# Performance work log

Hardware: AMD Instinct MI355X
Metric: run time of the kernel (lower is better)

Reference implementation:

```python
import jax, jax.numpy as jnp
import numpy as np

B, T, C = 128, 512, 512
EPS = 1e-5


def setup_inputs() -> dict:
    key = jax.random.key(0)
    ks = jax.random.split(key, 12)
    s_tri = 1.0 / np.sqrt(T)   # rough torch Linear init scale (per-row fan-in varies; fixed for simplicity)
    s_fc1 = 1.0 / np.sqrt(C)
    s_fc2 = 1.0 / np.sqrt(2 * C)
    return {
        "inputs": jax.random.normal(ks[0], (B, T, C), dtype=jnp.float32),
        "ln1_w": jnp.ones((T, C), jnp.float32),
        "ln1_b": jnp.zeros((T, C), jnp.float32),
        "ln2_w": jnp.ones((T, C), jnp.float32),
        "ln2_b": jnp.zeros((T, C), jnp.float32),
        # Row s of triu_W corresponds to nn.Linear(s+1, 1); entries j> s are masked in reference().
        "triu_W": jax.random.uniform(ks[1], (T, T), jnp.float32, -s_tri, s_tri),
        "triu_b": jax.random.uniform(ks[2], (T,), jnp.float32, -s_tri, s_tri),
        "fc1_W": jax.random.uniform(ks[3], (2 * C, C), jnp.float32, -s_fc1, s_fc1),
        "fc1_b": jax.random.uniform(ks[4], (2 * C,), jnp.float32, -s_fc1, s_fc1),
        "fc2_W": jax.random.uniform(ks[5], (C, 2 * C), jnp.float32, -s_fc2, s_fc2),
        "fc2_b": jax.random.uniform(ks[6], (C,), jnp.float32, -s_fc2, s_fc2),
    }


def _layernorm_2d(x, w, b):
    # torch nn.LayerNorm((T, C)): normalize jointly over the last TWO dims.
    mu = jnp.mean(x, axis=(-2, -1), keepdims=True)
    var = jnp.var(x, axis=(-2, -1), keepdims=True)
    return (x - mu) * jax.lax.rsqrt(var + EPS) * w + b


def reference(inputs, ln1_w, ln1_b, ln2_w, ln2_b, triu_W, triu_b, fc1_W, fc1_b, fc2_W, fc2_b):
    x = _layernorm_2d(inputs, ln1_w, ln1_b)                       # [B,T,C]
    # TriU time mixer on x.mT ([B,C,T]): out[..., s] = sum_{t<=s} W[s,t]*x[..., t] + b[s]
    Wm = jnp.tril(triu_W)                                          # causal mask
    xm = jnp.einsum('btc,st->bsc', x, Wm) + triu_b[None, :, None]  # [B,T,C] (already back-transposed)
    x2 = _layernorm_2d(xm + inputs, ln2_w, ln2_b)                  # [B,T,C]
    h = jax.nn.gelu(jnp.einsum('btc,hc->bth', x2, fc1_W) + fc1_b, approximate=False)
    y = jnp.einsum('bth,ch->btc', h, fc2_W) + fc2_b
    return x2 + y
```

## Files before the change

### kernel.cpp

```cpp
#include <hip/hip_runtime.h>
#include <hip/hip_fp8.h>
#include <cstdint>

typedef unsigned short u16;
typedef unsigned char u8;
typedef __attribute__((ext_vector_type(8))) short s16x8;
typedef __attribute__((ext_vector_type(4))) float f32x4;
typedef __attribute__((ext_vector_type(8))) unsigned short u16x8;
typedef __attribute__((ext_vector_type(4))) unsigned short u16x4;
typedef __attribute__((ext_vector_type(2))) long l64x2;

#define B_ 128
#define T_ 512
#define C_ 512
#define TC 262144

static __device__ __forceinline__ float bf2f(u16 u) {
  union { unsigned int i; float f; } v; v.i = ((unsigned int)u) << 16; return v.f;
}
static __device__ __forceinline__ u16 f2bf(float f) {
  union { float fv; unsigned int i; } v; v.fv = f;
  unsigned int r = (v.i + 0x7FFFu + ((v.i >> 16) & 1u)) >> 16;
  return (u16)r;
}
static __device__ __forceinline__ unsigned int cvtpk_fp8(float a, float b) {
  unsigned int r;
  asm volatile("v_cvt_pk_fp8_f32 %0, %1, %2" : "=v"(r) : "v"(a), "v"(b));
  return r & 0xffffu;
}
static __device__ __forceinline__ int kperm(int c) {
  return (c & ~63) | (((c >> 3) & 3) << 4) | (((c >> 5) & 1) << 3) | (c & 7);
}

static __device__ __forceinline__ float gelu_fast(float x) {
  float x2 = x * x;
  float arg = 1.5957691216057308f * x * fmaf(0.044715f, x2, 1.0f);
  return x / (1.0f + __expf(-arg));
}

#define GLD16(gp, lp) __builtin_amdgcn_global_load_lds( \
    (const __attribute__((address_space(1))) void*)(gp), \
    (__attribute__((address_space(3))) void*)(lp), 16, 0, 0)


__global__ __launch_bounds__(256)
void reduce_stats_kernel(const float* __restrict__ X, float2* __restrict__ partials,
                         u16* __restrict__ Xb,
                         const float* __restrict__ triu_W, u16* __restrict__ wmb,
                         const float* __restrict__ fc1_W, u8* __restrict__ w1f8,
                         const float* __restrict__ fc2_W, u8* __restrict__ w2f8) {
  const int b = blockIdx.y, blk = blockIdx.x, tid = threadIdx.x;
  const size_t gi = (size_t)b * TC + (size_t)blk * 2048 + (size_t)tid * 8;
  const float* p = X + gi;
  f32x4 v0 = *(const f32x4*)p;
  f32x4 v1 = *(const f32x4*)(p + 4);
  float s = 0.f, q = 0.f;
  u16x8 ob;
#pragma unroll
  for (int i = 0; i < 4; ++i) {
    s += v0[i] + v1[i]; q += v0[i] * v0[i] + v1[i] * v1[i];
    ob[i] = f2bf(v0[i]); ob[4 + i] = f2bf(v1[i]);
  }
  *(u16x8*)(Xb + gi) = ob;

  const int flat = (b * 128 + blk) * 256 + tid;
  if (flat < T_ * T_) {
    const int sr = flat >> 9, tcol = flat & 511;
    wmb[flat] = f2bf(tcol <= sr ? triu_W[flat] : 0.f);
  }
  if (flat < C_ * C_) {
    const int e = flat * 2;
    float2 a1 = *(const float2*)(fc1_W + e);
    float2 a2 = *(const float2*)(fc2_W + e);
    const int r1 = e >> 9,  c1 = e & 511;
    const int r2 = e >> 10, c2 = e & 1023;
    *(u16*)(w1f8 + (size_t)r1 * 512 + kperm(c1))  = (u16)cvtpk_fp8(a1.x, a1.y);
    *(u16*)(w2f8 + (size_t)r2 * 1024 + kperm(c2)) = (u16)cvtpk_fp8(a2.x, a2.y);
  }

  for (int o = 32; o; o >>= 1) { s += __shfl_down(s, o); q += __shfl_down(q, o); }
  __shared__ float ss[4], qq[4];
  if ((tid & 63) == 0) { ss[tid >> 6] = s; qq[tid >> 6] = q; }
  __syncthreads();
  if (tid == 0)
    partials[(size_t)b * 128 + blk] =
        make_float2(ss[0] + ss[1] + ss[2] + ss[3], qq[0] + qq[1] + qq[2] + qq[3]);
}


__global__ __launch_bounds__(256)
void ln1_transpose_kernel(const u16* __restrict__ Xb, const float* __restrict__ W,
                          const float* __restrict__ Bv, const float2* __restrict__ partials,
                          u16* __restrict__ xT) {
  const int b = blockIdx.z;
  const int t0 = blockIdx.y * 64, c0 = blockIdx.x * 64;
  const int tid = threadIdx.x;
  __shared__ u16 tile[64][72];
  __shared__ float smu, srs;

  if (tid < 64) {
    float2 p0 = partials[(size_t)b * 128 + tid];
    float2 p1 = partials[(size_t)b * 128 + 64 + tid];
    float s = p0.x + p1.x, q = p0.y + p1.y;
    for (int o = 32; o; o >>= 1) { s += __shfl_down(s, o); q += __shfl_down(q, o); }
    if (tid == 0) {
      float mean = s * (1.f / (float)TC);
      float var = q * (1.f / (float)TC) - mean * mean;
      smu = mean; srs = rsqrtf(var + 1e-5f);
    }
  }
  __syncthreads();
  const float mu = smu, rs = srs;

  const int rr = tid >> 4;
  const int cc = (tid & 15) * 4;
#pragma unroll
  for (int i = 0; i < 4; ++i) {
    const int lt = i * 16 + rr;
    const size_t wi = (size_t)(t0 + lt) * C_ + c0 + cc;
    u16x4 xa = *(const u16x4*)(Xb + (size_t)b * TC + wi);
    f32x4 w = *(const f32x4*)(W + wi);
    f32x4 bb = *(const f32x4*)(Bv + wi);
#pragma unroll
    for (int j = 0; j < 4; ++j)
      tile[lt][cc + j] = f2bf((bf2f(xa[j]) - mu) * rs * w[j] + bb[j]);
  }
  __syncthreads();
  const int c = tid >> 2;
  const int tg = (tid & 3) * 16;
  u16 buf[16];
#pragma unroll
  for (int i = 0; i < 16; ++i) buf[i] = tile[tg + i][c];
  const size_t o = (size_t)b * TC + (size_t)(c0 + c) * T_ + t0 + tg;
  u16x8 o0, o1;
#pragma unroll
  for (int i = 0; i < 8; ++i) { o0[i] = buf[i]; o1[i] = buf[8 + i]; }
  *(u16x8*)(xT + o) = o0;
  *(u16x8*)(xT + o + 8) = o1;
}


__global__ __launch_bounds__(256)
void ln2_apply_kernel(const u16* __restrict__ S, const float* __restrict__ W,
                      const float* __restrict__ Bv, const float2* __restrict__ partials2,
                      u16* __restrict__ x2, u8* __restrict__ x8) {
  const size_t i = ((size_t)blockIdx.x * 256 + threadIdx.x) * 8;
  const int b = (int)(i >> 18);
  const size_t r = i & (size_t)(TC - 1);
  float2 p0 = partials2[(size_t)b * 4 + 0];
  float2 p1 = partials2[(size_t)b * 4 + 1];
  float2 p2 = partials2[(size_t)b * 4 + 2];
  float2 p3 = partials2[(size_t)b * 4 + 3];
  float s = (p0.x + p1.x) + (p2.x + p3.x);
  float q = (p0.y + p1.y) + (p2.y + p3.y);
  const float mu = s * (1.f / (float)TC);
  const float rs = rsqrtf(q * (1.f / (float)TC) - mu * mu + 1e-5f);

  u16x8 sv = *(const u16x8*)(S + i);
  f32x4 w0 = *(const f32x4*)(W + r);
  f32x4 w1 = *(const f32x4*)(W + r + 4);
  f32x4 b0 = *(const f32x4*)(Bv + r);
  f32x4 b1 = *(const f32x4*)(Bv + r + 4);
  u16x8 o;
  float v[8];
#pragma unroll
  for (int j = 0; j < 4; ++j) {
    v[j]     = (bf2f(sv[j])     - mu) * rs * w0[j] + b0[j];
    v[4 + j] = (bf2f(sv[4 + j]) - mu) * rs * w1[j] + b1[j];
    o[j] = f2bf(v[j]); o[4 + j] = f2bf(v[4 + j]);
  }
  *(u16x8*)(x2 + i) = o;
  uint2 pk;
  pk.x = cvtpk_fp8(v[0], v[1]) | (cvtpk_fp8(v[2], v[3]) << 16);
  pk.y = cvtpk_fp8(v[4], v[5]) | (cvtpk_fp8(v[6], v[7]) << 16);
  const size_t pi = (i & ~(size_t)63) | (size_t)(((i >> 3) & 3) << 4) | (size_t)(((i >> 5) & 1) << 3);
  *(uint2*)(x8 + pi) = pk;
}


template <int MODE>
__global__ __launch_bounds__(512, (MODE == 0) ? 1 : 2)
void gemm_bt_kernel(const u16* __restrict__ A, const u16* __restrict__ Bm,
                    int K, int lda, int ldb,
                    void* __restrict__ Cp, int ldc,
                    const float* __restrict__ bias,
                    const void* __restrict__ res,
                    long long strideB, long long strideC,
                    float2* __restrict__ stat_part) {
  constexpr int TILE_U16 = (MODE == 0) ? 16384 : 8192;
  __shared__ u16 Asb[2 * TILE_U16];
  __shared__ u16 Bsb[2 * TILE_U16];
  __shared__ float rs_[8], rq_[8];
  const int tid = threadIdx.x;

  const int nwg = gridDim.x;
  const int orig = blockIdx.x;
  const int swz = (orig & 7) * (nwg >> 3) + (orig >> 3);
  int bx, by, bz;
  if (MODE == 0) { bz = swz >> 2; by = (swz >> 1) & 1; bx = swz & 1; }
  else if (MODE == 1) { bz = 0; by = swz >> 2; bx = swz & 3; }
  else { bz = 0; by = swz >> 1; bx = swz & 1; }

  const u16* Bp = Bm + (size_t)bz * (size_t)strideB;
  const int m0 = by * 256, n0 = bx * 256;
  int kTiles = K >> 6;
  if (MODE == 0) { const int need = (by + 1) * 4; if (need < kTiles) kTiles = need; }

  const int lane = tid & 63;
  const int wave = tid >> 6;
  const int wm = (wave >> 2) * 128;
  const int wn = (wave & 3) * 64;
  const int lr = lane & 15;
  const int kg = lane >> 4;

  f32x4 acc[8][4];
  const f32x4 zero = {0.f, 0.f, 0.f, 0.f};
#pragma unroll
  for (int m = 0; m < 8; ++m)
#pragma unroll
    for (int n = 0; n < 4; ++n) acc[m][n] = zero;

  auto STAGE_A = [&](int t) {
    const int k0 = t << 6;
    const int d = (t & 1) * 16384;
#pragma unroll
    for (int p = 0; p < 4; ++p) {
      const int q = p * 512 + tid;
      const int r = q >> 3;
      const int kcs = (q & 7) ^ (r & 7);
      GLD16(A + (size_t)(m0 + r) * lda + k0 + (kcs << 3), &Asb[d + q * 8]);
    }
  };
  auto STAGE_B = [&](int t) {
    const int k0 = t << 6;
    const int d = (t & 1) * 16384;
#pragma unroll
    for (int p = 0; p < 4; ++p) {
      const int q = p * 512 + tid;
      const int r = q >> 3;
      const int kcs = (q & 7) ^ (r & 7);
      GLD16(Bp + (size_t)(n0 + r) * ldb + k0 + (kcs << 3), &Bsb[d + q * 8]);
    }
  };
  auto STAGE_A8 = [&](int t) {
    const int k0 = t << 6;
    u8* lds = (u8*)Asb + (t & 1) * 16384;
    const u8* src = (const u8*)A;
#pragma unroll
    for (int p = 0; p < 2; ++p) {
      const int q = p * 512 + tid;
      const int lrow = q >> 3;
      const int cp = (q & 7) ^ (lrow & 7);
      const int dr = lrow + ((cp & 4) << 5);
      GLD16(src + (size_t)(m0 + dr) * lda + k0 + ((cp & 3) << 4), lds + q * 16);
    }
  };
  auto STAGE_B8 = [&](int t) {
    const int k0 = t << 6;
    u8* lds = (u8*)Bsb + (t & 1) * 16384;
    const u8* src = (const u8*)Bp;
#pragma unroll
    for (int p = 0; p < 2; ++p) {
      const int q = p * 512 + tid;
      const int lrow = q >> 3;
      const int cp = (q & 7) ^ (lrow & 7);
      const int dr = lrow + ((cp & 4) << 5);
      GLD16(src + (size_t)(n0 + dr) * ldb + k0 + ((cp & 3) << 4), lds + q * 16);
    }
  };

  if (MODE == 0) {
    STAGE_A(0); STAGE_B(0); STAGE_A(1);
    for (int kt = 0; kt < kTiles; ++kt) {
      const int d = (kt & 1) * 16384;
      if (kt + 1 < kTiles) asm volatile("s_waitcnt vmcnt(4)" ::: "memory");
      else                 asm volatile("s_waitcnt vmcnt(0)" ::: "memory");
      __builtin_amdgcn_s_barrier();
      asm volatile("" ::: "memory");

      s16x8 a0[8], a1[8], b0[4], b1[4];
#pragma unroll
      for (int m = 0; m < 8; ++m) {
        const int row = wm + m * 16 + lr;
        const u16* base = &Asb[d + row * 64];
        a0[m] = *(const s16x8*)(base + (((kg)     ^ (row & 7)) << 3));
        a1[m] = *(const s16x8*)(base + (((4 + kg) ^ (row & 7)) << 3));
      }
#pragma unroll
      for (int n = 0; n < 4; ++n) {
        const int row = wn + n * 16 + lr;
        b0[n] = *(const s16x8*)(&Bsb[d + row * 64] + (((kg) ^ (row & 7)) << 3));
      }
      if (kt + 1 < kTiles) STAGE_B(kt + 1);

      __builtin_amdgcn_s_setprio(1);
#pragma unroll
      for (int m = 0; m < 8; ++m)
#pragma unroll
        for (int n = 0; n < 4; ++n)
          acc[m][n] = __builtin_amdgcn_mfma_f32_16x16x32_bf16(a0[m], b0[n], acc[m][n], 0, 0, 0);
      __builtin_amdgcn_s_setprio(0);

#pragma unroll
      for (int n = 0; n < 4; ++n) {
        const int row = wn + n * 16 + lr;
        b1[n] = *(const s16x8*)(&Bsb[d + row * 64] + (((4 + kg) ^ (row & 7)) << 3));
      }
      asm volatile("s_waitcnt lgkmcnt(0)" ::: "memory");
      __builtin_amdgcn_s_barrier();
      asm volatile("" ::: "memory");
      if (kt + 2 < kTiles) STAGE_A(kt + 2);

      __builtin_amdgcn_s_setprio(1);
#pragma unroll
      for (int m = 0; m < 8; ++m)
#pragma unroll
        for (int n = 0; n < 4; ++n)
          acc[m][n] = __builtin_amdgcn_mfma_f32_16x16x32_bf16(a1[m], b1[n], acc[m][n], 0, 0, 0);
      __builtin_amdgcn_s_setprio(0);
    }
  } else {
    STAGE_A8(0); STAGE_B8(0); STAGE_A8(1);
    for (int kt = 0; kt < kTiles; ++kt) {
      const u8* Ad = (const u8*)Asb + (kt & 1) * 16384;
      const u8* Bd = (const u8*)Bsb + (kt & 1) * 16384;
      if (kt + 1 < kTiles) asm volatile("s_waitcnt vmcnt(2)" ::: "memory");
      else                 asm volatile("s_waitcnt vmcnt(0)" ::: "memory");
      __builtin_amdgcn_s_barrier();
      asm volatile("" ::: "memory");

      l64x2 av[8], bv[4];
#pragma unroll
      for (int m = 0; m < 8; ++m) {
        const int dd = wm + m * 16 + lr;
        const int lrow = dd & 127;
        const int q = (((dd >> 7) << 2) | kg) ^ (lrow & 7);
        av[m] = *(const l64x2*)(Ad + lrow * 128 + (q << 4));
      }
#pragma unroll
      for (int n = 0; n < 4; ++n) {
        const int dd = wn + n * 16 + lr;
        const int lrow = dd & 127;
        const int q = (((dd >> 7) << 2) | kg) ^ (lrow & 7);
        bv[n] = *(const l64x2*)(Bd + lrow * 128 + (q << 4));
      }
      if (kt + 1 < kTiles) STAGE_B8(kt + 1);

      asm volatile("s_waitcnt lgkmcnt(0)" ::: "memory");
      __builtin_amdgcn_s_setprio(1);
#pragma unroll
      for (int m = 0; m < 8; ++m)
#pragma unroll
        for (int n = 0; n < 4; ++n)
          acc[m][n] = __builtin_amdgcn_mfma_f32_16x16x32_fp8_fp8(av[m][0], bv[n][0], acc[m][n], 0, 0, 0);
      __builtin_amdgcn_s_setprio(0);

      __builtin_amdgcn_s_barrier();
      asm volatile("" ::: "memory");
      if (kt + 2 < kTiles) STAGE_A8(kt + 2);

      __builtin_amdgcn_s_setprio(1);
#pragma unroll
      for (int m = 0; m < 8; ++m)
#pragma unroll
        for (int n = 0; n < 4; ++n)
          acc[m][n] = __builtin_amdgcn_mfma_f32_16x16x32_fp8_fp8(av[m][1], bv[n][1], acc[m][n], 0, 0, 0);
      __builtin_amdgcn_s_setprio(0);
    }
  }

  if (MODE == 0) {
    u16* Cptr = (u16*)Cp + (size_t)bz * (size_t)strideC;
    const u16* inp = (const u16*)res + (size_t)bz * (size_t)strideC;
    float psum = 0.f, psq = 0.f;
#pragma unroll
    for (int m = 0; m < 8; ++m) {
      const int rb = m0 + wm + m * 16 + kg * 4;
#pragma unroll
      for (int n = 0; n < 4; ++n) {
        const int col = n0 + wn + n * 16 + lr;
#pragma unroll
        for (int j = 0; j < 4; ++j) {
          const size_t idx = (size_t)(rb + j) * ldc + col;
          float v = acc[m][n][j] + bf2f(inp[idx]) + bias[rb + j];
          psum += v; psq += v * v;
          Cptr[idx] = f2bf(v);
        }
      }
    }
    for (int o = 32; o; o >>= 1) { psum += __shfl_down(psum, o); psq += __shfl_down(psq, o); }
    if (lane == 0) { rs_[wave] = psum; rq_[wave] = psq; }
    __syncthreads();
    if (tid == 0) {
      float s = 0.f, q = 0.f;
#pragma unroll
      for (int w = 0; w < 8; ++w) { s += rs_[w]; q += rq_[w]; }
      stat_part[(size_t)bz * 4 + by * 2 + bx] = make_float2(s, q);
    }
  } else if (MODE == 1) {
    u8* Cptr = (u8*)Cp;
#pragma unroll
    for (int m = 0; m < 8; ++m) {
      const int rb = m0 + wm + m * 16 + kg * 4;
#pragma unroll
      for (int n = 0; n < 4; ++n) {
        const int col = n0 + wn + n * 16 + lr;
        const float bs = bias[col];
        const int pcol = kperm(col);
        unsigned int p01 = cvtpk_fp8(gelu_fast(acc[m][n][0] + bs),
                                     gelu_fast(acc[m][n][1] + bs));
        unsigned int p23 = cvtpk_fp8(gelu_fast(acc[m][n][2] + bs),
                                     gelu_fast(acc[m][n][3] + bs));
        Cptr[(size_t)(rb + 0) * ldc + pcol] = (u8)(p01 & 0xff);
        Cptr[(size_t)(rb + 1) * ldc + pcol] = (u8)(p01 >> 8);
        Cptr[(size_t)(rb + 2) * ldc + pcol] = (u8)(p23 & 0xff);
        Cptr[(size_t)(rb + 3) * ldc + pcol] = (u8)(p23 >> 8);
      }
    }
  } else {
    float* Cptr = (float*)Cp;
    const u16* x2p = (const u16*)res;
#pragma unroll
    for (int m = 0; m < 8; ++m) {
      const int rb = m0 + wm + m * 16 + kg * 4;
#pragma unroll
      for (int n = 0; n < 4; ++n) {
        const int col = n0 + wn + n * 16 + lr;
        const float bs = bias[col];
#pragma unroll
        for (int j = 0; j < 4; ++j) {
          const size_t idx = (size_t)(rb + j) * ldc + col;
          Cptr[idx] = acc[m][n][j] + bs + bf2f(x2p[idx]);
        }
      }
    }
  }
}


extern "C" void kernel_launch(void* const* d_in, const int* in_sizes, int n_in,
                              void* d_out, int out_size, void* d_ws, size_t ws_size,
                              hipStream_t stream) {
  const float* inputs = (const float*)d_in[0];
  const float* ln1_w  = (const float*)d_in[1];
  const float* ln1_b  = (const float*)d_in[2];
  const float* ln2_w  = (const float*)d_in[3];
  const float* ln2_b  = (const float*)d_in[4];
  const float* triu_W = (const float*)d_in[5];
  const float* triu_b = (const float*)d_in[6];
  const float* fc1_W  = (const float*)d_in[7];
  const float* fc1_b  = (const float*)d_in[8];
  const float* fc2_W  = (const float*)d_in[9];
  const float* fc2_b  = (const float*)d_in[10];
  float* out = (float*)d_out;
  (void)in_sizes; (void)n_in; (void)out_size; (void)ws_size;

  char* ws = (char*)d_ws;
  size_t off = 0;
  auto carve = [&](size_t bytes) {
    char* p = ws + off;
    off += (bytes + 255) & ~(size_t)255;
    return p;
  };
  u16* s_bf = (u16*)carve((size_t)B_ * T_ * C_ * 2);
  u16* xT   = (u16*)carve((size_t)B_ * T_ * C_ * 2);
  u16* x2   = xT;
  u16* inb  = (u16*)carve((size_t)B_ * T_ * C_ * 2);
  u8*  x8   = (u8*)carve((size_t)B_ * T_ * C_);
  u8*  h    = (u8*)carve((size_t)B_ * T_ * 2 * C_);
  u16* wmb  = (u16*)carve((size_t)T_ * T_ * 2);
  u8*  w1f8 = (u8*)carve((size_t)2 * C_ * C_);
  u8*  w2f8 = (u8*)carve((size_t)C_ * 2 * C_);
  float2* partials  = (float2*)carve(128 * 128 * sizeof(float2));
  float2* partials2 = (float2*)carve(128 * 4 * sizeof(float2));

  reduce_stats_kernel<<<dim3(128, 128), 256, 0, stream>>>(
      inputs, partials, inb, triu_W, wmb, fc1_W, w1f8, fc2_W, w2f8);
  ln1_transpose_kernel<<<dim3(8, 8, 128), 256, 0, stream>>>(inb, ln1_w, ln1_b, partials, xT);
  gemm_bt_kernel<0><<<512, 512, 0, stream>>>(
      wmb, xT, 512, 512, 512, s_bf, 512, triu_b, inb, (long long)TC, (long long)TC, partials2);
  ln2_apply_kernel<<<16384, 256, 0, stream>>>(s_bf, ln2_w, ln2_b, partials2, x2, x8);
  gemm_bt_kernel<1><<<1024, 512, 0, stream>>>(
      (const u16*)x8, (const u16*)w1f8, 512, 512, 512, h, 1024, fc1_b, nullptr, 0, 0, nullptr);
  gemm_bt_kernel<2><<<512, 512, 0, stream>>>(
      (const u16*)h, (const u16*)w2f8, 1024, 1024, 1024, out, 512, fc2_b, x2, 0, 0, nullptr);
}
```

Before: 337.6 us.

## Recompute LN2 output in fc2 epilogue instead of storing bf16 x2

The ln2 apply kernel no longer writes a bf16 copy of the normalized activations. The fc2 GEMM epilogue now reads the pre-norm sum, rebuilds the per-batch mean and rstd from the partial stats, and reapplies the LN2 weight and bias for the residual. This removes one full-tensor bf16 write, at the cost of extra weight and bias loads and arithmetic in the epilogue. It also moves the LDS wait in the fp8 GEMM loop to after the MFMA block, which could let the fragment reads overlap the matrix math.

```diff
diff --git a/kernel.cpp b/kernel.cpp
--- a/kernel.cpp
+++ b/kernel.cpp
@@ -143,7 +143,7 @@
 __global__ __launch_bounds__(256)
 void ln2_apply_kernel(const u16* __restrict__ S, const float* __restrict__ W,
                       const float* __restrict__ Bv, const float2* __restrict__ partials2,
-                      u16* __restrict__ x2, u8* __restrict__ x8) {
+                      u8* __restrict__ x8) {
   const size_t i = ((size_t)blockIdx.x * 256 + threadIdx.x) * 8;
   const int b = (int)(i >> 18);
   const size_t r = i & (size_t)(TC - 1);
@@ -161,15 +161,12 @@
   f32x4 w1 = *(const f32x4*)(W + r + 4);
   f32x4 b0 = *(const f32x4*)(Bv + r);
   f32x4 b1 = *(const f32x4*)(Bv + r + 4);
-  u16x8 o;
   float v[8];
 #pragma unroll
   for (int j = 0; j < 4; ++j) {
     v[j]     = (bf2f(sv[j])     - mu) * rs * w0[j] + b0[j];
     v[4 + j] = (bf2f(sv[4 + j]) - mu) * rs * w1[j] + b1[j];
-    o[j] = f2bf(v[j]); o[4 + j] = f2bf(v[4 + j]);
-  }
-  *(u16x8*)(x2 + i) = o;
+  }
   uint2 pk;
   pk.x = cvtpk_fp8(v[0], v[1]) | (cvtpk_fp8(v[2], v[3]) << 16);
   pk.y = cvtpk_fp8(v[4], v[5]) | (cvtpk_fp8(v[6], v[7]) << 16);
@@ -180,13 +177,14 @@
 
 template <int MODE>
 __global__ __launch_bounds__(512, (MODE == 0) ? 1 : 2)
-void gemm_bt_kernel(const u16* __restrict__ A, const u16* __restrict__ Bm,
+void gemm_bt_kernel(const void* __restrict__ Av, const void* __restrict__ Bmv,
                     int K, int lda, int ldb,
                     void* __restrict__ Cp, int ldc,
                     const float* __restrict__ bias,
                     const void* __restrict__ res,
                     long long strideB, long long strideC,
-                    float2* __restrict__ stat_part) {
+                    float2* __restrict__ stat_part,
+                    const float* __restrict__ ln2w, const float* __restrict__ ln2b) {
   constexpr int TILE_U16 = (MODE == 0) ? 16384 : 8192;
   __shared__ u16 Asb[2 * TILE_U16];
   __shared__ u16 Bsb[2 * TILE_U16];
@@ -201,7 +199,6 @@
   else if (MODE == 1) { bz = 0; by = swz >> 2; bx = swz & 3; }
   else { bz = 0; by = swz >> 1; bx = swz & 1; }
 
-  const u16* Bp = Bm + (size_t)bz * (size_t)strideB;
   const int m0 = by * 256, n0 = bx * 256;
   int kTiles = K >> 6;
   if (MODE == 0) { const int need = (by + 1) * 4; if (need < kTiles) kTiles = need; }
@@ -220,56 +217,31 @@
 #pragma unroll
     for (int n = 0; n < 4; ++n) acc[m][n] = zero;
 
-  auto STAGE_A = [&](int t) {
-    const int k0 = t << 6;
-    const int d = (t & 1) * 16384;
-#pragma unroll
-    for (int p = 0; p < 4; ++p) {
-      const int q = p * 512 + tid;
-      const int r = q >> 3;
-      const int kcs = (q & 7) ^ (r & 7);
-      GLD16(A + (size_t)(m0 + r) * lda + k0 + (kcs << 3), &Asb[d + q * 8]);
-    }
-  };
-  auto STAGE_B = [&](int t) {
-    const int k0 = t << 6;
-    const int d = (t & 1) * 16384;
-#pragma unroll
-    for (int p = 0; p < 4; ++p) {
-      const int q = p * 512 + tid;
-      const int r = q >> 3;
-      const int kcs = (q & 7) ^ (r & 7);
-      GLD16(Bp + (size_t)(n0 + r) * ldb + k0 + (kcs << 3), &Bsb[d + q * 8]);
-    }
-  };
-  auto STAGE_A8 = [&](int t) {
-    const int k0 = t << 6;
-    u8* lds = (u8*)Asb + (t & 1) * 16384;
-    const u8* src = (const u8*)A;
-#pragma unroll
-    for (int p = 0; p < 2; ++p) {
-      const int q = p * 512 + tid;
-      const int lrow = q >> 3;
-      const int cp = (q & 7) ^ (lrow & 7);
-      const int dr = lrow + ((cp & 4) << 5);
-      GLD16(src + (size_t)(m0 + dr) * lda + k0 + ((cp & 3) << 4), lds + q * 16);
-    }
-  };
-  auto STAGE_B8 = [&](int t) {
-    const int k0 = t << 6;
-    u8* lds = (u8*)Bsb + (t & 1) * 16384;
-    const u8* src = (const u8*)Bp;
-#pragma unroll
-    for (int p = 0; p < 2; ++p) {
-      const int q = p * 512 + tid;
-      const int lrow = q >> 3;
-      const int cp = (q & 7) ^ (lrow & 7);
-      const int dr = lrow + ((cp & 4) << 5);
-      GLD16(src + (size_t)(n0 + dr) * ldb + k0 + ((cp & 3) << 4), lds + q * 16);
-    }
-  };
-
   if (MODE == 0) {
+    const u16* A = (const u16*)Av;
+    const u16* Bp = (const u16*)Bmv + (size_t)bz * (size_t)strideB;
+    auto STAGE_A = [&](int t) {
+      const int k0 = t << 6;
+      const int d = (t & 1) * 16384;
+#pragma unroll
+      for (int p = 0; p < 4; ++p) {
+        const int q = p * 512 + tid;
+        const int r = q >> 3;
+        const int kcs = (q & 7) ^ (r & 7);
+        GLD16(A + (size_t)(m0 + r) * lda + k0 + (kcs << 3), &Asb[d + q * 8]);
+      }
+    };
+    auto STAGE_B = [&](int t) {
+      const int k0 = t << 6;
+      const int d = (t & 1) * 16384;
+#pragma unroll
+      for (int p = 0; p < 4; ++p) {
+        const int q = p * 512 + tid;
+        const int r = q >> 3;
+        const int kcs = (q & 7) ^ (r & 7);
+        GLD16(Bp + (size_t)(n0 + r) * ldb + k0 + (kcs << 3), &Bsb[d + q * 8]);
+      }
+    };
     STAGE_A(0); STAGE_B(0); STAGE_A(1);
     for (int kt = 0; kt < kTiles; ++kt) {
       const int d = (kt & 1) * 16384;
@@ -320,6 +292,32 @@
       __builtin_amdgcn_s_setprio(0);
     }
   } else {
+    const u8* A = (const u8*)Av;
+    const u8* Bp = (const u8*)Bmv;
+    auto STAGE_A8 = [&](int t) {
+      const int k0 = t << 6;
+      u8* lds = (u8*)Asb + (t & 1) * 16384;
+#pragma unroll
+      for (int p = 0; p < 2; ++p) {
+        const int q = p * 512 + tid;
+        const int lrow = q >> 3;
+        const int cp = (q & 7) ^ (lrow & 7);
+        const int dr = lrow + ((cp & 4) << 5);
+        GLD16(A + (size_t)(m0 + dr) * lda + k0 + ((cp & 3) << 4), lds + q * 16);
+      }
+    };
+    auto STAGE_B8 = [&](int t) {
+      const int k0 = t << 6;
+      u8* lds = (u8*)Bsb + (t & 1) * 16384;
+#pragma unroll
+      for (int p = 0; p < 2; ++p) {
+        const int q = p * 512 + tid;
+        const int lrow = q >> 3;
+        const int cp = (q & 7) ^ (lrow & 7);
+        const int dr = lrow + ((cp & 4) << 5);
+        GLD16(Bp + (size_t)(n0 + dr) * ldb + k0 + ((cp & 3) << 4), lds + q * 16);
+      }
+    };
     STAGE_A8(0); STAGE_B8(0); STAGE_A8(1);
     for (int kt = 0; kt < kTiles; ++kt) {
       const u8* Ad = (const u8*)Asb + (kt & 1) * 16384;
@@ -346,7 +344,6 @@
       }
       if (kt + 1 < kTiles) STAGE_B8(kt + 1);
 
-      asm volatile("s_waitcnt lgkmcnt(0)" ::: "memory");
       __builtin_amdgcn_s_setprio(1);
 #pragma unroll
       for (int m = 0; m < 8; ++m)
@@ -355,6 +352,7 @@
           acc[m][n] = __builtin_amdgcn_mfma_f32_16x16x32_fp8_fp8(av[m][0], bv[n][0], acc[m][n], 0, 0, 0);
       __builtin_amdgcn_s_setprio(0);
 
+      asm volatile("s_waitcnt lgkmcnt(0)" ::: "memory");
       __builtin_amdgcn_s_barrier();
       asm volatile("" ::: "memory");
       if (kt + 2 < kTiles) STAGE_A8(kt + 2);
@@ -419,7 +417,16 @@
     }
   } else {
     float* Cptr = (float*)Cp;
-    const u16* x2p = (const u16*)res;
+    const u16* sp = (const u16*)res;
+    const int bb = m0 >> 9;
+    float2 p0 = stat_part[(size_t)bb * 4 + 0];
+    float2 p1 = stat_part[(size_t)bb * 4 + 1];
+    float2 p2 = stat_part[(size_t)bb * 4 + 2];
+    float2 p3 = stat_part[(size_t)bb * 4 + 3];
+    float ssum = (p0.x + p1.x) + (p2.x + p3.x);
+    float sq = (p0.y + p1.y) + (p2.y + p3.y);
+    const float mu = ssum * (1.f / (float)TC);
+    const float rsv = rsqrtf(sq * (1.f / (float)TC) - mu * mu + 1e-5f);
 #pragma unroll
     for (int m = 0; m < 8; ++m) {
       const int rb = m0 + wm + m * 16 + kg * 4;
@@ -430,7 +437,9 @@
 #pragma unroll
         for (int j = 0; j < 4; ++j) {
           const size_t idx = (size_t)(rb + j) * ldc + col;
-          Cptr[idx] = acc[m][n][j] + bs + bf2f(x2p[idx]);
+          const int wi = (int)(idx & (size_t)(TC - 1));
+          float x2v = (bf2f(sp[idx]) - mu) * rsv * ln2w[wi] + ln2b[wi];
+          Cptr[idx] = acc[m][n][j] + bs + x2v;
         }
       }
     }
@@ -464,7 +473,6 @@
   };
   u16* s_bf = (u16*)carve((size_t)B_ * T_ * C_ * 2);
   u16* xT   = (u16*)carve((size_t)B_ * T_ * C_ * 2);
-  u16* x2   = xT;
   u16* inb  = (u16*)carve((size_t)B_ * T_ * C_ * 2);
   u8*  x8   = (u8*)carve((size_t)B_ * T_ * C_);
   u8*  h    = (u8*)carve((size_t)B_ * T_ * 2 * C_);
@@ -478,10 +486,11 @@
       inputs, partials, inb, triu_W, wmb, fc1_W, w1f8, fc2_W, w2f8);
   ln1_transpose_kernel<<<dim3(8, 8, 128), 256, 0, stream>>>(inb, ln1_w, ln1_b, partials, xT);
   gemm_bt_kernel<0><<<512, 512, 0, stream>>>(
-      wmb, xT, 512, 512, 512, s_bf, 512, triu_b, inb, (long long)TC, (long long)TC, partials2);
-  ln2_apply_kernel<<<16384, 256, 0, stream>>>(s_bf, ln2_w, ln2_b, partials2, x2, x8);
+      wmb, xT, 512, 512, 512, s_bf, 512, triu_b, inb,
+      (long long)TC, (long long)TC, partials2, nullptr, nullptr);
+  ln2_apply_kernel<<<16384, 256, 0, stream>>>(s_bf, ln2_w, ln2_b, partials2, x8);
   gemm_bt_kernel<1><<<1024, 512, 0, stream>>>(
-      (const u16*)x8, (const u16*)w1f8, 512, 512, 512, h, 1024, fc1_b, nullptr, 0, 0, nullptr);
+      x8, w1f8, 512, 512, 512, h, 1024, fc1_b, nullptr, 0, 0, nullptr, nullptr, nullptr);
   gemm_bt_kernel<2><<<512, 512, 0, stream>>>(
-      (const u16*)h, (const u16*)w2f8, 1024, 1024, 1024, out, 512, fc2_b, x2, 0, 0, nullptr);
-}
+      h, w2f8, 1024, 1024, 1024, out, 512, fc2_b, s_bf, 0, 0, partials2, ln2_w, ln2_b);
+}
```

Measured after the change: 352.6 us. +4.4%, slower.
